# Kernel tuning notes

Measured on AMD Instinct MI355X. Metric: run time of the kernel, lower is better.

The kernel has to match this reference:

```python
import jax, jax.numpy as jnp
import numpy as np

ALPHA = 1.702  # ORT swiglu activation constant


def setup_inputs() -> dict:
    key = jax.random.key(0)
    ks = jax.random.split(key, 6)
    B, S, H, I, E = 4, 1024, 2048, 2048, 8
    return {
        "hidden_states": jax.random.normal(ks[0], (B, S, H), dtype=jnp.float32),
        "gate_w": jax.random.normal(ks[1], (E, H), dtype=jnp.float32) * 0.02,
        "fc1_w": jax.random.normal(ks[2], (E, 2 * I, H), dtype=jnp.float32) * 0.02,
        "fc1_b": jax.random.normal(ks[3], (E, 2 * I), dtype=jnp.float32) * 0.02,
        "fc2_w": jax.random.normal(ks[4], (E, H, I), dtype=jnp.float32) * 0.02,
        "fc2_b": jax.random.normal(ks[5], (E, H), dtype=jnp.float32) * 0.02,
        "top_k": 2,
    }


def reference(hidden_states, gate_w, fc1_w, fc1_b, fc2_w, fc2_b, top_k):
    B, S, H = hidden_states.shape
    E = gate_w.shape[0]
    x = hidden_states.reshape(-1, H)                      # [T, H]
    T = x.shape[0]

    # Router: softmax -> top-k -> renormalize selected weights
    logits = jnp.einsum("th,eh->te", x, gate_w)           # [T, E]
    probs = jax.nn.softmax(logits, axis=-1)
    top_vals, top_idx = jax.lax.top_k(probs, top_k)       # [T, k]
    top_vals = top_vals / jnp.sum(top_vals, axis=-1, keepdims=True)
    # Dense combine weights [T, E] (zero for non-selected experts)
    combine = jnp.zeros((T, E), dtype=x.dtype).at[
        jnp.arange(T)[:, None], top_idx
    ].add(top_vals)

    # Expert FC1 (packed gate/linear, interleaved) -> swiglu -> FC2
    h = jnp.einsum("th,efh->etf", x, fc1_w) + fc1_b[:, None, :]   # [E, T, 2I]
    g = h[..., 0::2]                                              # gate part [E, T, I]
    l = h[..., 1::2]                                              # linear part [E, T, I]
    a = g * jax.nn.sigmoid(ALPHA * g) * (l + 1.0)                 # [E, T, I]
    y = jnp.einsum("eti,ehi->eth", a, fc2_w) + fc2_b[:, None, :]  # [E, T, H]

    out = jnp.einsum("te,eth->th", combine, y)            # weighted combine
    return out.reshape(B, S, H)
```

## Files before the change

### kernel.cpp

```cpp
#include <hip/hip_runtime.h>
#include <math.h>


#define T_TOK 4096
#define H_DIM 2048
#define I_DIM 2048
#define F_DIM 4096
#define E_NUM 8
#define ALPHA_C 1.702f

#define TILE_M 64
#define KT 32
#define ACT_CAP_F (2 * T_TOK + E_NUM * TILE_M)
#define BTM 128
#define ACT_CAP_B (2 * T_TOK + E_NUM * BTM)

typedef unsigned short ushort_t;
typedef __attribute__((ext_vector_type(8))) unsigned short ushort8v;
typedef __attribute__((ext_vector_type(8))) __bf16 bf16x8;
typedef __attribute__((ext_vector_type(4))) float f32x4;

__device__ __forceinline__ ushort_t f2bf(float f) {
    unsigned int u = __float_as_uint(f);
    unsigned int r = (u + 0x7FFFu + ((u >> 16) & 1u)) >> 16;
    return (ushort_t)r;
}
__device__ __forceinline__ float bf2f(ushort_t b) {
    return __uint_as_float(((unsigned int)b) << 16);
}

__device__ __forceinline__ void gl_lds16(const ushort_t* g, ushort_t* l) {
    __builtin_amdgcn_global_load_lds(
        (const __attribute__((address_space(1))) void*)g,
        (__attribute__((address_space(3))) void*)l, 16, 0, 0);
}

__global__ __launch_bounds__(256) void cvt_kernel(
    const float4* __restrict__ in, ushort4* __restrict__ out, int n4) {
    int idx = blockIdx.x * 256 + threadIdx.x;
    int stride = gridDim.x * 256;
    for (int i = idx; i < n4; i += stride) {
        float4 v = in[i];
        out[i] = make_ushort4(f2bf(v.x), f2bf(v.y), f2bf(v.z), f2bf(v.w));
    }
}

__global__ __launch_bounds__(64) void gate_kernel(
    const float* __restrict__ x, const float* __restrict__ gw,
    int* __restrict__ tok, float* __restrict__ wgt,
    int4* __restrict__ tidx, float2* __restrict__ twgt,
    int* __restrict__ cnt) {
    int t = blockIdx.x;
    int lane = threadIdx.x;
    const float* xr = x + (size_t)t * H_DIM;
    float acc[E_NUM];
#pragma unroll
    for (int e = 0; e < E_NUM; e++) acc[e] = 0.f;
    for (int j = lane; j < H_DIM; j += 64) {
        float xv = xr[j];
#pragma unroll
        for (int e = 0; e < E_NUM; e++) acc[e] += xv * gw[e * H_DIM + j];
    }
#pragma unroll
    for (int e = 0; e < E_NUM; e++) {
#pragma unroll
        for (int s = 32; s > 0; s >>= 1) acc[e] += __shfl_xor(acc[e], s, 64);
    }
    if (lane == 0) {
        int i0 = 0; float b0 = acc[0];
        for (int e = 1; e < E_NUM; e++) if (acc[e] > b0) { b0 = acc[e]; i0 = e; }
        int i1 = -1; float b1 = -3.0e38f;
        for (int e = 0; e < E_NUM; e++) {
            if (e == i0) continue;
            if (acc[e] > b1) { b1 = acc[e]; i1 = e; }
        }
        float e10 = expf(b1 - b0);
        float w0 = 1.f / (1.f + e10);
        float w1 = 1.f - w0;
        int p0 = atomicAdd(&cnt[i0], 1);
        tok[i0 * T_TOK + p0] = t; wgt[i0 * T_TOK + p0] = w0;
        int p1 = atomicAdd(&cnt[i1], 1);
        tok[i1 * T_TOK + p1] = t; wgt[i1 * T_TOK + p1] = w1;
        tidx[t] = make_int4(i0, p0, i1, p1);
        twgt[t] = make_float2(w0, w1);
    }
}

__global__ __launch_bounds__(256) void pad_kernel(
    int* __restrict__ tok, float* __restrict__ wgt,
    const int* __restrict__ cnt, int* __restrict__ cnt_pad,
    int* __restrict__ off, int tile) {
    __shared__ int s_cnt[E_NUM], s_pad[E_NUM];
    if (threadIdx.x == 0) {
        int o = 0;
        for (int e = 0; e < E_NUM; e++) {
            int c = cnt[e];
            int cp = (c + tile - 1) / tile * tile;
            s_cnt[e] = c; s_pad[e] = cp;
            cnt_pad[e] = cp;
            off[e] = o;
            o += cp;
        }
    }
    __syncthreads();
    for (int e = 0; e < E_NUM; e++) {
        for (int p = s_cnt[e] + (int)threadIdx.x; p < s_pad[e]; p += 256) {
            tok[e * T_TOK + p] = 0;
            wgt[e * T_TOK + p] = 0.f;
        }
    }
}

__global__ __launch_bounds__(256, 3) void fc1_mfma(
    const ushort_t* __restrict__ xb, const ushort_t* __restrict__ w1b,
    const float* __restrict__ b1, const int* __restrict__ tok,
    const int* __restrict__ cnt_pad, const int* __restrict__ off,
    ushort_t* __restrict__ act) {
    int e = blockIdx.y >> 5;
    int tile = blockIdx.y & 31;
    if (tile * BTM >= cnt_pad[e]) return;
    int i0 = blockIdx.x * 64;

    __shared__ ushort_t As[128 * 32];
    __shared__ ushort_t Bg[64 * 32];
    __shared__ ushort_t Bl[64 * 32];

    int tid = threadIdx.x;
    int lane = tid & 63;
    int ww = tid >> 6;
    int wm = ww & 1, wn = ww >> 1;
    int l15 = lane & 15, quad = lane >> 4;
    int koff = (lane & 3) * 8;

    const int* tlist = tok + e * T_TOK + tile * BTM;
    int ar0 = ww * 32 + (lane >> 2);
    const ushort_t* asrc0 = xb + (size_t)tlist[ar0] * H_DIM + koff;
    const ushort_t* asrc1 = xb + (size_t)tlist[ar0 + 16] * H_DIM + koff;
    int il = ww * 16 + (lane >> 2);
    const ushort_t* bsrc = w1b + ((size_t)e * F_DIM + 2 * (i0 + il)) * H_DIM + koff;

    ushort_t* adst0 = As + (ww * 32) * 32;
    ushort_t* adst1 = As + (ww * 32 + 16) * 32;
    ushort_t* bgdst = Bg + (ww * 16) * 32;
    ushort_t* bldst = Bl + (ww * 16) * 32;

    f32x4 zf = {0.f, 0.f, 0.f, 0.f};
    f32x4 accg[4][2], accl[4][2];
#pragma unroll
    for (int mc = 0; mc < 4; mc++)
#pragma unroll
        for (int nc = 0; nc < 2; nc++) { accg[mc][nc] = zf; accl[mc][nc] = zf; }

    for (int k0 = 0; k0 < H_DIM; k0 += 32) {
        __syncthreads();
        gl_lds16(asrc0, adst0);
        gl_lds16(asrc1, adst1);
        gl_lds16(bsrc, bgdst);
        gl_lds16(bsrc + H_DIM, bldst);
        asrc0 += 32; asrc1 += 32; bsrc += 32;
        __syncthreads();

        bf16x8 af[4], bgf[2], blf[2];
#pragma unroll
        for (int mc = 0; mc < 4; mc++)
            af[mc] = *(const bf16x8*)&As[(wm * 64 + mc * 16 + l15) * 32 + quad * 8];
#pragma unroll
        for (int nc = 0; nc < 2; nc++) {
            bgf[nc] = *(const bf16x8*)&Bg[(wn * 32 + nc * 16 + l15) * 32 + quad * 8];
            blf[nc] = *(const bf16x8*)&Bl[(wn * 32 + nc * 16 + l15) * 32 + quad * 8];
        }
#pragma unroll
        for (int mc = 0; mc < 4; mc++)
#pragma unroll
            for (int nc = 0; nc < 2; nc++) {
                accg[mc][nc] = __builtin_amdgcn_mfma_f32_16x16x32_bf16(
                    af[mc], bgf[nc], accg[mc][nc], 0, 0, 0);
                accl[mc][nc] = __builtin_amdgcn_mfma_f32_16x16x32_bf16(
                    af[mc], blf[nc], accl[mc][nc], 0, 0, 0);
            }
    }

    int rowbase = off[e] + tile * BTM + wm * 64;
    int colbase = i0 + wn * 32;
    float bgc[2], blc[2];
#pragma unroll
    for (int nc = 0; nc < 2; nc++) {
        int i = colbase + nc * 16 + l15;
        bgc[nc] = b1[(size_t)e * F_DIM + 2 * i];
        blc[nc] = b1[(size_t)e * F_DIM + 2 * i + 1];
    }
#pragma unroll
    for (int mc = 0; mc < 4; mc++)
#pragma unroll
        for (int nc = 0; nc < 2; nc++) {
            int i = colbase + nc * 16 + l15;
#pragma unroll
            for (int r = 0; r < 4; r++) {
                int m = rowbase + mc * 16 + quad * 4 + r;
                float g = accg[mc][nc][r] + bgc[nc];
                float l = accl[mc][nc][r] + blc[nc];
                float s = 1.f / (1.f + expf(-ALPHA_C * g));
                act[(size_t)m * I_DIM + i] = f2bf(g * s * (l + 1.f));
            }
        }
}

__global__ __launch_bounds__(256, 3) void fc2_mfma(
    const ushort_t* __restrict__ act, const ushort_t* __restrict__ w2b,
    const float* __restrict__ b2, const int* __restrict__ cnt_pad,
    const int* __restrict__ off, ushort_t* __restrict__ ybuf) {
    int e = blockIdx.y >> 5;
    int tile = blockIdx.y & 31;
    if (tile * BTM >= cnt_pad[e]) return;
    int h0 = blockIdx.x * 128;
    int rowbase = off[e] + tile * BTM;

    __shared__ ushort_t As[128 * 32];
    __shared__ ushort_t Bs[128 * 32];

    int tid = threadIdx.x;
    int lane = tid & 63;
    int ww = tid >> 6;
    int wm = ww & 1, wn = ww >> 1;
    int l15 = lane & 15, quad = lane >> 4;
    int koff = (lane & 3) * 8;

    int ar = ww * 32 + (lane >> 2);
    const ushort_t* asrc0 = act + (size_t)(rowbase + ar) * I_DIM + koff;
    const ushort_t* asrc1 = asrc0 + (size_t)16 * I_DIM;
    const ushort_t* bsrc0 = w2b + ((size_t)e * H_DIM + h0 + ar) * I_DIM + koff;
    const ushort_t* bsrc1 = bsrc0 + (size_t)16 * I_DIM;

    ushort_t* adst0 = As + (ww * 32) * 32;
    ushort_t* adst1 = As + (ww * 32 + 16) * 32;
    ushort_t* bdst0 = Bs + (ww * 32) * 32;
    ushort_t* bdst1 = Bs + (ww * 32 + 16) * 32;

    f32x4 zf = {0.f, 0.f, 0.f, 0.f};
    f32x4 acc[4][4];
#pragma unroll
    for (int mc = 0; mc < 4; mc++)
#pragma unroll
        for (int nc = 0; nc < 4; nc++) acc[mc][nc] = zf;

    for (int k0 = 0; k0 < I_DIM; k0 += 32) {
        __syncthreads();
        gl_lds16(asrc0, adst0);
        gl_lds16(asrc1, adst1);
        gl_lds16(bsrc0, bdst0);
        gl_lds16(bsrc1, bdst1);
        asrc0 += 32; asrc1 += 32; bsrc0 += 32; bsrc1 += 32;
        __syncthreads();

        bf16x8 af[4], bf[4];
#pragma unroll
        for (int mc = 0; mc < 4; mc++)
            af[mc] = *(const bf16x8*)&As[(wm * 64 + mc * 16 + l15) * 32 + quad * 8];
#pragma unroll
        for (int nc = 0; nc < 4; nc++)
            bf[nc] = *(const bf16x8*)&Bs[(wn * 64 + nc * 16 + l15) * 32 + quad * 8];
#pragma unroll
        for (int mc = 0; mc < 4; mc++)
#pragma unroll
            for (int nc = 0; nc < 4; nc++)
                acc[mc][nc] = __builtin_amdgcn_mfma_f32_16x16x32_bf16(
                    af[mc], bf[nc], acc[mc][nc], 0, 0, 0);
    }

    float bc[4];
#pragma unroll
    for (int nc = 0; nc < 4; nc++)
        bc[nc] = b2[(size_t)e * H_DIM + h0 + wn * 64 + nc * 16 + l15];
#pragma unroll
    for (int mc = 0; mc < 4; mc++)
#pragma unroll
        for (int nc = 0; nc < 4; nc++) {
            int h = h0 + wn * 64 + nc * 16 + l15;
#pragma unroll
            for (int r = 0; r < 4; r++) {
                int m = rowbase + wm * 64 + mc * 16 + quad * 4 + r;
                ybuf[(size_t)m * H_DIM + h] = f2bf(acc[mc][nc][r] + bc[nc]);
            }
        }
}

__global__ __launch_bounds__(256) void combine_kernel(
    const ushort_t* __restrict__ ybuf, const int4* __restrict__ tidx,
    const float2* __restrict__ twgt, const int* __restrict__ off,
    float* __restrict__ out) {
    int t = blockIdx.x;
    int4 idx = tidx[t];
    float2 w = twgt[t];
    size_t r0 = (size_t)off[idx.x] + idx.y;
    size_t r1 = (size_t)off[idx.z] + idx.w;
    int h = threadIdx.x * 8;
    ushort8v a = *(const ushort8v*)(ybuf + r0 * H_DIM + h);
    ushort8v b = *(const ushort8v*)(ybuf + r1 * H_DIM + h);
    float* op = out + (size_t)t * H_DIM + h;
#pragma unroll
    for (int q = 0; q < 8; q++)
        op[q] = w.x * bf2f(a[q]) + w.y * bf2f(b[q]);
}

__global__ __launch_bounds__(256) void fc1_kernel(
    const float* __restrict__ x, const float* __restrict__ w1,
    const float* __restrict__ b1, const int* __restrict__ tok,
    const int* __restrict__ cnt_pad, const int* __restrict__ off,
    ushort_t* __restrict__ act) {
    int e = blockIdx.y >> 6;
    int tile = blockIdx.y & 63;
    if (tile * TILE_M >= cnt_pad[e]) return;
    int i0 = blockIdx.x * 64;
    int f0 = i0 * 2;

    __shared__ float xs[KT][TILE_M + 4];
    __shared__ float wsh[KT][128 + 4];

    int tid = threadIdx.x;
    int tx = tid & 15, ty = tid >> 4;
    int rloc = tid >> 3;
    int c4 = (tid & 7) * 4;

    const int* tlist = tok + e * T_TOK + tile * TILE_M;
    int tk0 = tlist[rloc];
    int tk1 = tlist[rloc + 32];
    const float* xp0 = x + (size_t)tk0 * H_DIM + c4;
    const float* xp1 = x + (size_t)tk1 * H_DIM + c4;
    const float* wp = w1 + ((size_t)e * F_DIM + f0 + rloc) * H_DIM + c4;

    float ga[4][4] = {{0.f}}, la[4][4] = {{0.f}};

    for (int k0 = 0; k0 < H_DIM; k0 += KT) {
        __syncthreads();
        {
            float4 v0 = *(const float4*)(xp0 + k0);
            float4 v1 = *(const float4*)(xp1 + k0);
            xs[c4 + 0][rloc] = v0.x; xs[c4 + 1][rloc] = v0.y;
            xs[c4 + 2][rloc] = v0.z; xs[c4 + 3][rloc] = v0.w;
            xs[c4 + 0][rloc + 32] = v1.x; xs[c4 + 1][rloc + 32] = v1.y;
            xs[c4 + 2][rloc + 32] = v1.z; xs[c4 + 3][rloc + 32] = v1.w;
        }
        {
#pragma unroll
            for (int r = 0; r < 4; r++) {
                float4 v = *(const float4*)(wp + (size_t)(32 * r) * H_DIM + k0);
                int fr = rloc + 32 * r;
                wsh[c4 + 0][fr] = v.x; wsh[c4 + 1][fr] = v.y;
                wsh[c4 + 2][fr] = v.z; wsh[c4 + 3][fr] = v.w;
            }
        }
        __syncthreads();
#pragma unroll
        for (int k = 0; k < KT; k++) {
            float4 xv = *(const float4*)&xs[k][ty * 4];
            float4 wa = *(const float4*)&wsh[k][tx * 8];
            float4 wb = *(const float4*)&wsh[k][tx * 8 + 4];
            float xm[4] = {xv.x, xv.y, xv.z, xv.w};
            float gg[4] = {wa.x, wa.z, wb.x, wb.z};
            float ll[4] = {wa.y, wa.w, wb.y, wb.w};
#pragma unroll
            for (int m = 0; m < 4; m++)
#pragma unroll
                for (int n = 0; n < 4; n++) {
                    ga[m][n] += xm[m] * gg[n];
                    la[m][n] += xm[m] * ll[n];
                }
        }
    }

    int rowbase = off[e] + tile * TILE_M;
    float bg[4], bl[4];
#pragma unroll
    for (int n = 0; n < 4; n++) {
        int i = i0 + tx * 4 + n;
        bg[n] = b1[(size_t)e * F_DIM + 2 * i];
        bl[n] = b1[(size_t)e * F_DIM + 2 * i + 1];
    }
#pragma unroll
    for (int m = 0; m < 4; m++) {
        int row = rowbase + ty * 4 + m;
        ushort_t us[4];
#pragma unroll
        for (int n = 0; n < 4; n++) {
            float g = ga[m][n] + bg[n];
            float l = la[m][n] + bl[n];
            float s = 1.f / (1.f + expf(-ALPHA_C * g));
            us[n] = f2bf(g * s * (l + 1.f));
        }
        *(ushort4*)&act[(size_t)row * I_DIM + i0 + tx * 4] =
            make_ushort4(us[0], us[1], us[2], us[3]);
    }
}

__global__ __launch_bounds__(256) void fc2_kernel(
    const ushort_t* __restrict__ act, const float* __restrict__ w2,
    const float* __restrict__ b2, const int* __restrict__ tok,
    const float* __restrict__ wgt, const int* __restrict__ cnt_pad,
    const int* __restrict__ off, float* __restrict__ out) {
    int e = blockIdx.y >> 6;
    int tile = blockIdx.y & 63;
    if (tile * TILE_M >= cnt_pad[e]) return;
    int h0 = blockIdx.x * 64;

    __shared__ float as_[KT][TILE_M + 4];
    __shared__ float wsh[KT][64 + 4];

    int tid = threadIdx.x;
    int tx = tid & 15, ty = tid >> 4;
    int rowbase = off[e] + tile * TILE_M;

    int arow = tid >> 2;
    int ac8 = (tid & 3) * 8;
    const ushort_t* ap = act + (size_t)(rowbase + arow) * I_DIM + ac8;
    int rloc = tid >> 3;
    int c4 = (tid & 7) * 4;
    const float* wp = w2 + ((size_t)e * H_DIM + h0 + rloc) * I_DIM + c4;

    float acc[4][4] = {{0.f}};

    for (int k0 = 0; k0 < I_DIM; k0 += KT) {
        __syncthreads();
        {
            ushort8v v = *(const ushort8v*)(ap + k0);
#pragma unroll
            for (int q = 0; q < 8; q++) as_[ac8 + q][arow] = bf2f(v[q]);
        }
        {
#pragma unroll
            for (int r = 0; r < 2; r++) {
                float4 v = *(const float4*)(wp + (size_t)(32 * r) * I_DIM + k0);
                int hr = rloc + 32 * r;
                wsh[c4 + 0][hr] = v.x; wsh[c4 + 1][hr] = v.y;
                wsh[c4 + 2][hr] = v.z; wsh[c4 + 3][hr] = v.w;
            }
        }
        __syncthreads();
#pragma unroll
        for (int k = 0; k < KT; k++) {
            float4 xv = *(const float4*)&as_[k][ty * 4];
            float4 wv = *(const float4*)&wsh[k][tx * 4];
            float xm[4] = {xv.x, xv.y, xv.z, xv.w};
            float wn[4] = {wv.x, wv.y, wv.z, wv.w};
#pragma unroll
            for (int m = 0; m < 4; m++)
#pragma unroll
                for (int n = 0; n < 4; n++) acc[m][n] += xm[m] * wn[n];
        }
    }

    const int* tlist = tok + e * T_TOK + tile * TILE_M;
    const float* wlist = wgt + e * T_TOK + tile * TILE_M;
#pragma unroll
    for (int m = 0; m < 4; m++) {
        int row = ty * 4 + m;
        int t = tlist[row];
        float w = wlist[row];
        if (w == 0.f) continue;
#pragma unroll
        for (int n = 0; n < 4; n++) {
            int h = h0 + tx * 4 + n;
            float y = acc[m][n] + b2[(size_t)e * H_DIM + h];
            atomicAdd(out + (size_t)t * H_DIM + h, w * y);
        }
    }
}

extern "C" void kernel_launch(void* const* d_in, const int* in_sizes, int n_in,
                              void* d_out, int out_size, void* d_ws, size_t ws_size,
                              hipStream_t stream) {
    const float* x  = (const float*)d_in[0];
    const float* gw = (const float*)d_in[1];
    const float* w1 = (const float*)d_in[2];
    const float* b1 = (const float*)d_in[3];
    const float* w2 = (const float*)d_in[4];
    const float* b2 = (const float*)d_in[5];
    float* out = (float*)d_out;
    char* ws = (char*)d_ws;

    size_t w1b_sz = (size_t)E_NUM * F_DIM * H_DIM * 2;
    size_t w2b_sz = (size_t)E_NUM * H_DIM * I_DIM * 2;
    size_t xb_sz  = (size_t)T_TOK * H_DIM * 2;
    size_t act_sz = (size_t)ACT_CAP_B * I_DIM * 2;
    size_t tok_sz = (size_t)E_NUM * T_TOK * 4;
    size_t tidx_sz = (size_t)T_TOK * 16;
    size_t twgt_sz = (size_t)T_TOK * 8;
    size_t need_big = w1b_sz + w2b_sz + xb_sz + act_sz + 2 * tok_sz +
                      tidx_sz + twgt_sz + 64;

    if (ws_size >= need_big) {
        ushort_t* w1b = (ushort_t*)ws;
        ushort_t* w2b = (ushort_t*)(ws + w1b_sz);
        ushort_t* xb  = (ushort_t*)(ws + w1b_sz + w2b_sz);
        ushort_t* act = (ushort_t*)(ws + w1b_sz + w2b_sz + xb_sz);
        char* p = ws + w1b_sz + w2b_sz + xb_sz + act_sz;
        int*    tok  = (int*)p;                 p += tok_sz;
        float*  wgt  = (float*)p;               p += tok_sz;
        int4*   tidx = (int4*)p;                p += tidx_sz;
        float2* twgt = (float2*)p;              p += twgt_sz;
        int*    cnt  = (int*)p;
        int*    cnt_pad = cnt + E_NUM;
        int*    off  = cnt_pad + E_NUM;
        ushort_t* ybuf = w1b;

        hipMemsetAsync(cnt, 0, E_NUM * sizeof(int), stream);
        cvt_kernel<<<8192, 256, 0, stream>>>(
            (const float4*)w1, (ushort4*)w1b, (int)(w1b_sz / 8));
        cvt_kernel<<<8192, 256, 0, stream>>>(
            (const float4*)w2, (ushort4*)w2b, (int)(w2b_sz / 8));
        cvt_kernel<<<2048, 256, 0, stream>>>(
            (const float4*)x, (ushort4*)xb, (int)(xb_sz / 8));
        gate_kernel<<<T_TOK, 64, 0, stream>>>(x, gw, tok, wgt, tidx, twgt, cnt);
        pad_kernel<<<1, 256, 0, stream>>>(tok, wgt, cnt, cnt_pad, off, BTM);
        fc1_mfma<<<dim3(I_DIM / 64, E_NUM * 32), 256, 0, stream>>>(
            xb, w1b, b1, tok, cnt_pad, off, act);
        fc2_mfma<<<dim3(H_DIM / 128, E_NUM * 32), 256, 0, stream>>>(
            act, w2b, b2, cnt_pad, off, ybuf);
        combine_kernel<<<T_TOK, 256, 0, stream>>>(ybuf, tidx, twgt, off, out);
        return;
    }

    size_t actB = (size_t)ACT_CAP_F * I_DIM * 2;
    ushort_t* act = (ushort_t*)ws;
    char* p = ws + actB;
    int*    tok  = (int*)p;     p += tok_sz;
    float*  wgt  = (float*)p;   p += tok_sz;
    int4*   tidx = (int4*)p;    p += tidx_sz;
    float2* twgt = (float2*)p;  p += twgt_sz;
    int*    cnt  = (int*)p;
    int*    cnt_pad = cnt + E_NUM;
    int*    off  = cnt_pad + E_NUM;
    size_t need = actB + 2 * tok_sz + tidx_sz + twgt_sz + 64;
    if (ws_size < need) return;

    hipMemsetAsync(cnt, 0, E_NUM * sizeof(int), stream);
    hipMemsetAsync(d_out, 0, (size_t)T_TOK * H_DIM * sizeof(float), stream);
    gate_kernel<<<T_TOK, 64, 0, stream>>>(x, gw, tok, wgt, tidx, twgt, cnt);
    pad_kernel<<<1, 256, 0, stream>>>(tok, wgt, cnt, cnt_pad, off, TILE_M);
    fc1_kernel<<<dim3(I_DIM / 64, E_NUM * 64), 256, 0, stream>>>(
        x, w1, b1, tok, cnt_pad, off, act);
    fc2_kernel<<<dim3(H_DIM / 64, E_NUM * 64), 256, 0, stream>>>(
        act, w2, b2, tok, wgt, cnt_pad, off, out);
}
```

Before: 916.8 us.

## Fuse weight conversions, fold x conversion into gate, widen GEMM K-step

Merges the two weight fp32-to-bf16 conversion launches into one kernel with 16-byte stores, and folds the activation conversion into a vectorised gate kernel that handles four tokens per block. Both MFMA GEMMs now load a 64-wide K slab per barrier pair, halving the number of synchronisations. The sigmoid uses the hardware exp2 and reciprocal intrinsics. The cost is doubled LDS per block, which may reduce occupancy, and a small accuracy change in the sigmoid.

```diff
diff --git a/kernel.cpp b/kernel.cpp
--- a/kernel.cpp
+++ b/kernel.cpp
@@ -8,6 +8,7 @@
 #define F_DIM 4096
 #define E_NUM 8
 #define ALPHA_C 1.702f
+#define ALPHA_LOG2E 2.4554674f
 
 #define TILE_M 64
 #define KT 32
@@ -35,31 +36,47 @@
         (__attribute__((address_space(3))) void*)l, 16, 0, 0);
 }
 
-__global__ __launch_bounds__(256) void cvt_kernel(
-    const float4* __restrict__ in, ushort4* __restrict__ out, int n4) {
+__global__ __launch_bounds__(256) void cvt_w(
+    const float* __restrict__ w1, const float* __restrict__ w2,
+    ushort_t* __restrict__ dst, int n1g, int ntg) {
     int idx = blockIdx.x * 256 + threadIdx.x;
     int stride = gridDim.x * 256;
-    for (int i = idx; i < n4; i += stride) {
-        float4 v = in[i];
-        out[i] = make_ushort4(f2bf(v.x), f2bf(v.y), f2bf(v.z), f2bf(v.w));
-    }
-}
-
-__global__ __launch_bounds__(64) void gate_kernel(
+    for (int i = idx; i < ntg; i += stride) {
+        const float* s = (i < n1g) ? (w1 + (size_t)i * 8)
+                                   : (w2 + ((size_t)(i - n1g)) * 8);
+        float4 v0 = *(const float4*)s;
+        float4 v1 = *(const float4*)(s + 4);
+        ushort8v o;
+        o[0] = f2bf(v0.x); o[1] = f2bf(v0.y); o[2] = f2bf(v0.z); o[3] = f2bf(v0.w);
+        o[4] = f2bf(v1.x); o[5] = f2bf(v1.y); o[6] = f2bf(v1.z); o[7] = f2bf(v1.w);
+        *(ushort8v*)(dst + (size_t)i * 8) = o;
+    }
+}
+
+__global__ __launch_bounds__(256) void gate_kernel(
     const float* __restrict__ x, const float* __restrict__ gw,
+    ushort_t* __restrict__ xb,
     int* __restrict__ tok, float* __restrict__ wgt,
     int4* __restrict__ tidx, float2* __restrict__ twgt,
     int* __restrict__ cnt) {
-    int t = blockIdx.x;
-    int lane = threadIdx.x;
+    int t = blockIdx.x * 4 + (threadIdx.x >> 6);
+    int lane = threadIdx.x & 63;
     const float* xr = x + (size_t)t * H_DIM;
+    ushort_t* xbr = xb + (size_t)t * H_DIM;
     float acc[E_NUM];
 #pragma unroll
     for (int e = 0; e < E_NUM; e++) acc[e] = 0.f;
-    for (int j = lane; j < H_DIM; j += 64) {
-        float xv = xr[j];
-#pragma unroll
-        for (int e = 0; e < E_NUM; e++) acc[e] += xv * gw[e * H_DIM + j];
+#pragma unroll
+    for (int i = 0; i < H_DIM / 256; i++) {
+        int j = (i * 64 + lane) * 4;
+        float4 xv = *(const float4*)(xr + j);
+        *(ushort4*)(xbr + j) =
+            make_ushort4(f2bf(xv.x), f2bf(xv.y), f2bf(xv.z), f2bf(xv.w));
+#pragma unroll
+        for (int e = 0; e < E_NUM; e++) {
+            float4 g = *(const float4*)(gw + e * H_DIM + j);
+            acc[e] += xv.x * g.x + xv.y * g.y + xv.z * g.z + xv.w * g.w;
+        }
     }
 #pragma unroll
     for (int e = 0; e < E_NUM; e++) {
@@ -121,28 +138,33 @@
     if (tile * BTM >= cnt_pad[e]) return;
     int i0 = blockIdx.x * 64;
 
-    __shared__ ushort_t As[128 * 32];
-    __shared__ ushort_t Bg[64 * 32];
-    __shared__ ushort_t Bl[64 * 32];
+    __shared__ ushort_t As[2][128 * 32];
+    __shared__ ushort_t Bg[2][64 * 32];
+    __shared__ ushort_t Bl[2][64 * 32];
 
     int tid = threadIdx.x;
     int lane = tid & 63;
     int ww = tid >> 6;
     int wm = ww & 1, wn = ww >> 1;
     int l15 = lane & 15, quad = lane >> 4;
+    int r4 = lane >> 2;
     int koff = (lane & 3) * 8;
 
     const int* tlist = tok + e * T_TOK + tile * BTM;
-    int ar0 = ww * 32 + (lane >> 2);
-    const ushort_t* asrc0 = xb + (size_t)tlist[ar0] * H_DIM + koff;
-    const ushort_t* asrc1 = xb + (size_t)tlist[ar0 + 16] * H_DIM + koff;
-    int il = ww * 16 + (lane >> 2);
+    int ar0 = ww * 32 + r4;
+    const ushort_t* a0 = xb + (size_t)tlist[ar0] * H_DIM + koff;
+    const ushort_t* a1 = xb + (size_t)tlist[ar0 + 16] * H_DIM + koff;
+    int il = ww * 16 + r4;
     const ushort_t* bsrc = w1b + ((size_t)e * F_DIM + 2 * (i0 + il)) * H_DIM + koff;
 
-    ushort_t* adst0 = As + (ww * 32) * 32;
-    ushort_t* adst1 = As + (ww * 32 + 16) * 32;
-    ushort_t* bgdst = Bg + (ww * 16) * 32;
-    ushort_t* bldst = Bl + (ww * 16) * 32;
+    ushort_t* ad0a = &As[0][(ww * 32) * 32];
+    ushort_t* ad0b = &As[0][(ww * 32 + 16) * 32];
+    ushort_t* ad1a = &As[1][(ww * 32) * 32];
+    ushort_t* ad1b = &As[1][(ww * 32 + 16) * 32];
+    ushort_t* bg0 = &Bg[0][(ww * 16) * 32];
+    ushort_t* bg1 = &Bg[1][(ww * 16) * 32];
+    ushort_t* bl0 = &Bl[0][(ww * 16) * 32];
+    ushort_t* bl1 = &Bl[1][(ww * 16) * 32];
 
     f32x4 zf = {0.f, 0.f, 0.f, 0.f};
     f32x4 accg[4][2], accl[4][2];
@@ -151,33 +173,40 @@
 #pragma unroll
         for (int nc = 0; nc < 2; nc++) { accg[mc][nc] = zf; accl[mc][nc] = zf; }
 
-    for (int k0 = 0; k0 < H_DIM; k0 += 32) {
-        __syncthreads();
-        gl_lds16(asrc0, adst0);
-        gl_lds16(asrc1, adst1);
-        gl_lds16(bsrc, bgdst);
-        gl_lds16(bsrc + H_DIM, bldst);
-        asrc0 += 32; asrc1 += 32; bsrc += 32;
-        __syncthreads();
-
-        bf16x8 af[4], bgf[2], blf[2];
-#pragma unroll
-        for (int mc = 0; mc < 4; mc++)
-            af[mc] = *(const bf16x8*)&As[(wm * 64 + mc * 16 + l15) * 32 + quad * 8];
-#pragma unroll
-        for (int nc = 0; nc < 2; nc++) {
-            bgf[nc] = *(const bf16x8*)&Bg[(wn * 32 + nc * 16 + l15) * 32 + quad * 8];
-            blf[nc] = *(const bf16x8*)&Bl[(wn * 32 + nc * 16 + l15) * 32 + quad * 8];
-        }
-#pragma unroll
-        for (int mc = 0; mc < 4; mc++)
+    for (int k0 = 0; k0 < H_DIM; k0 += 64) {
+        __syncthreads();
+        gl_lds16(a0, ad0a);
+        gl_lds16(a1, ad0b);
+        gl_lds16(a0 + 32, ad1a);
+        gl_lds16(a1 + 32, ad1b);
+        gl_lds16(bsrc, bg0);
+        gl_lds16(bsrc + 32, bg1);
+        gl_lds16(bsrc + H_DIM, bl0);
+        gl_lds16(bsrc + H_DIM + 32, bl1);
+        a0 += 64; a1 += 64; bsrc += 64;
+        __syncthreads();
+
+#pragma unroll
+        for (int kk = 0; kk < 2; kk++) {
+            bf16x8 af[4], bgf[2], blf[2];
+#pragma unroll
+            for (int mc = 0; mc < 4; mc++)
+                af[mc] = *(const bf16x8*)&As[kk][(wm * 64 + mc * 16 + l15) * 32 + quad * 8];
 #pragma unroll
             for (int nc = 0; nc < 2; nc++) {
-                accg[mc][nc] = __builtin_amdgcn_mfma_f32_16x16x32_bf16(
-                    af[mc], bgf[nc], accg[mc][nc], 0, 0, 0);
-                accl[mc][nc] = __builtin_amdgcn_mfma_f32_16x16x32_bf16(
-                    af[mc], blf[nc], accl[mc][nc], 0, 0, 0);
+                bgf[nc] = *(const bf16x8*)&Bg[kk][(wn * 32 + nc * 16 + l15) * 32 + quad * 8];
+                blf[nc] = *(const bf16x8*)&Bl[kk][(wn * 32 + nc * 16 + l15) * 32 + quad * 8];
             }
+#pragma unroll
+            for (int mc = 0; mc < 4; mc++)
+#pragma unroll
+                for (int nc = 0; nc < 2; nc++) {
+                    accg[mc][nc] = __builtin_amdgcn_mfma_f32_16x16x32_bf16(
+                        af[mc], bgf[nc], accg[mc][nc], 0, 0, 0);
+                    accl[mc][nc] = __builtin_amdgcn_mfma_f32_16x16x32_bf16(
+                        af[mc], blf[nc], accl[mc][nc], 0, 0, 0);
+                }
+        }
     }
 
     int rowbase = off[e] + tile * BTM + wm * 64;
@@ -199,7 +228,8 @@
                 int m = rowbase + mc * 16 + quad * 4 + r;
                 float g = accg[mc][nc][r] + bgc[nc];
                 float l = accl[mc][nc][r] + blc[nc];
-                float s = 1.f / (1.f + expf(-ALPHA_C * g));
+                float s = __builtin_amdgcn_rcpf(
+                    1.f + __builtin_amdgcn_exp2f(-ALPHA_LOG2E * g));
                 act[(size_t)m * I_DIM + i] = f2bf(g * s * (l + 1.f));
             }
         }
@@ -215,26 +245,31 @@
     int h0 = blockIdx.x * 128;
     int rowbase = off[e] + tile * BTM;
 
-    __shared__ ushort_t As[128 * 32];
-    __shared__ ushort_t Bs[128 * 32];
+    __shared__ ushort_t As[2][128 * 32];
+    __shared__ ushort_t Bs[2][128 * 32];
 
     int tid = threadIdx.x;
     int lane = tid & 63;
     int ww = tid >> 6;
     int wm = ww & 1, wn = ww >> 1;
     int l15 = lane & 15, quad = lane >> 4;
+    int r4 = lane >> 2;
     int koff = (lane & 3) * 8;
 
-    int ar = ww * 32 + (lane >> 2);
-    const ushort_t* asrc0 = act + (size_t)(rowbase + ar) * I_DIM + koff;
-    const ushort_t* asrc1 = asrc0 + (size_t)16 * I_DIM;
-    const ushort_t* bsrc0 = w2b + ((size_t)e * H_DIM + h0 + ar) * I_DIM + koff;
-    const ushort_t* bsrc1 = bsrc0 + (size_t)16 * I_DIM;
-
-    ushort_t* adst0 = As + (ww * 32) * 32;
-    ushort_t* adst1 = As + (ww * 32 + 16) * 32;
-    ushort_t* bdst0 = Bs + (ww * 32) * 32;
-    ushort_t* bdst1 = Bs + (ww * 32 + 16) * 32;
+    int ar = ww * 32 + r4;
+    const ushort_t* a0 = act + (size_t)(rowbase + ar) * I_DIM + koff;
+    const ushort_t* a1 = a0 + (size_t)16 * I_DIM;
+    const ushort_t* b0 = w2b + ((size_t)e * H_DIM + h0 + ar) * I_DIM + koff;
+    const ushort_t* b1p = b0 + (size_t)16 * I_DIM;
+
+    ushort_t* ad0a = &As[0][(ww * 32) * 32];
+    ushort_t* ad0b = &As[0][(ww * 32 + 16) * 32];
+    ushort_t* ad1a = &As[1][(ww * 32) * 32];
+    ushort_t* ad1b = &As[1][(ww * 32 + 16) * 32];
+    ushort_t* bd0a = &Bs[0][(ww * 32) * 32];
+    ushort_t* bd0b = &Bs[0][(ww * 32 + 16) * 32];
+    ushort_t* bd1a = &Bs[1][(ww * 32) * 32];
+    ushort_t* bd1b = &Bs[1][(ww * 32 + 16) * 32];
 
     f32x4 zf = {0.f, 0.f, 0.f, 0.f};
     f32x4 acc[4][4];
@@ -243,28 +278,35 @@
 #pragma unroll
         for (int nc = 0; nc < 4; nc++) acc[mc][nc] = zf;
 
-    for (int k0 = 0; k0 < I_DIM; k0 += 32) {
-        __syncthreads();
-        gl_lds16(asrc0, adst0);
-        gl_lds16(asrc1, adst1);
-        gl_lds16(bsrc0, bdst0);
-        gl_lds16(bsrc1, bdst1);
-        asrc0 += 32; asrc1 += 32; bsrc0 += 32; bsrc1 += 32;
-        __syncthreads();
-
-        bf16x8 af[4], bf[4];
-#pragma unroll
-        for (int mc = 0; mc < 4; mc++)
-            af[mc] = *(const bf16x8*)&As[(wm * 64 + mc * 16 + l15) * 32 + quad * 8];
-#pragma unroll
-        for (int nc = 0; nc < 4; nc++)
-            bf[nc] = *(const bf16x8*)&Bs[(wn * 64 + nc * 16 + l15) * 32 + quad * 8];
-#pragma unroll
-        for (int mc = 0; mc < 4; mc++)
+    for (int k0 = 0; k0 < I_DIM; k0 += 64) {
+        __syncthreads();
+        gl_lds16(a0, ad0a);
+        gl_lds16(a1, ad0b);
+        gl_lds16(a0 + 32, ad1a);
+        gl_lds16(a1 + 32, ad1b);
+        gl_lds16(b0, bd0a);
+        gl_lds16(b1p, bd0b);
+        gl_lds16(b0 + 32, bd1a);
+        gl_lds16(b1p + 32, bd1b);
+        a0 += 64; a1 += 64; b0 += 64; b1p += 64;
+        __syncthreads();
+
+#pragma unroll
+        for (int kk = 0; kk < 2; kk++) {
+            bf16x8 af[4], bf[4];
+#pragma unroll
+            for (int mc = 0; mc < 4; mc++)
+                af[mc] = *(const bf16x8*)&As[kk][(wm * 64 + mc * 16 + l15) * 32 + quad * 8];
 #pragma unroll
             for (int nc = 0; nc < 4; nc++)
-                acc[mc][nc] = __builtin_amdgcn_mfma_f32_16x16x32_bf16(
-                    af[mc], bf[nc], acc[mc][nc], 0, 0, 0);
+                bf[nc] = *(const bf16x8*)&Bs[kk][(wn * 64 + nc * 16 + l15) * 32 + quad * 8];
+#pragma unroll
+            for (int mc = 0; mc < 4; mc++)
+#pragma unroll
+                for (int nc = 0; nc < 4; nc++)
+                    acc[mc][nc] = __builtin_amdgcn_mfma_f32_16x16x32_bf16(
+                        af[mc], bf[nc], acc[mc][nc], 0, 0, 0);
+        }
     }
 
     float bc[4];
@@ -489,7 +531,6 @@
 
     if (ws_size >= need_big) {
         ushort_t* w1b = (ushort_t*)ws;
-        ushort_t* w2b = (ushort_t*)(ws + w1b_sz);
         ushort_t* xb  = (ushort_t*)(ws + w1b_sz + w2b_sz);
         ushort_t* act = (ushort_t*)(ws + w1b_sz + w2b_sz + xb_sz);
         char* p = ws + w1b_sz + w2b_sz + xb_sz + act_sz;
@@ -500,16 +541,16 @@
         int*    cnt  = (int*)p;
         int*    cnt_pad = cnt + E_NUM;
         int*    off  = cnt_pad + E_NUM;
+        ushort_t* w2b = (ushort_t*)(ws + w1b_sz);
         ushort_t* ybuf = w1b;
 
+        int n1g = (int)(w1b_sz / 16);
+        int ntg = n1g + (int)(w2b_sz / 16);
+
         hipMemsetAsync(cnt, 0, E_NUM * sizeof(int), stream);
-        cvt_kernel<<<8192, 256, 0, stream>>>(
-            (const float4*)w1, (ushort4*)w1b, (int)(w1b_sz / 8));
-        cvt_kernel<<<8192, 256, 0, stream>>>(
-            (const float4*)w2, (ushort4*)w2b, (int)(w2b_sz / 8));
-        cvt_kernel<<<2048, 256, 0, stream>>>(
-            (const float4*)x, (ushort4*)xb, (int)(xb_sz / 8));
-        gate_kernel<<<T_TOK, 64, 0, stream>>>(x, gw, tok, wgt, tidx, twgt, cnt);
+        cvt_w<<<4096, 256, 0, stream>>>(w1, w2, w1b, n1g, ntg);
+        gate_kernel<<<T_TOK / 4, 256, 0, stream>>>(
+            x, gw, xb, tok, wgt, tidx, twgt, cnt);
         pad_kernel<<<1, 256, 0, stream>>>(tok, wgt, cnt, cnt_pad, off, BTM);
         fc1_mfma<<<dim3(I_DIM / 64, E_NUM * 32), 256, 0, stream>>>(
             xb, w1b, b1, tok, cnt_pad, off, act);
@@ -534,7 +575,8 @@
 
     hipMemsetAsync(cnt, 0, E_NUM * sizeof(int), stream);
     hipMemsetAsync(d_out, 0, (size_t)T_TOK * H_DIM * sizeof(float), stream);
-    gate_kernel<<<T_TOK, 64, 0, stream>>>(x, gw, tok, wgt, tidx, twgt, cnt);
+    gate_kernel<<<T_TOK / 4, 256, 0, stream>>>(
+        x, gw, act , tok, wgt, tidx, twgt, cnt);
     pad_kernel<<<1, 256, 0, stream>>>(tok, wgt, cnt, cnt_pad, off, TILE_M);
     fc1_kernel<<<dim3(I_DIM / 64, E_NUM * 64), 256, 0, stream>>>(
         x, w1, b1, tok, cnt_pad, off, act);
```

Result: faster. 859.5 us (-6.2%).
